# Kernel optimization log

Hardware: AMD Instinct MI355X
Metric: run time of the kernel (lower is better)

Reference implementation:

```python
import jax, jax.numpy as jnp
import numpy as np
import math

D_MODEL = 1024
NUM_HEADS = 16
D_K = D_MODEL // NUM_HEADS
SEQ_LEN = 2048
THETA = 10000.0


def _rope_tables(seq_len, d_k, theta):
    # inv_freq over even dims, angles repeated-interleaved to full d_k
    inv_freq = theta ** (-jnp.arange(0, d_k, 2, dtype=jnp.float32) / d_k)  # [d_k/2]
    pos = jnp.arange(seq_len, dtype=jnp.float32)                          # [s]
    angles = pos[:, None] * inv_freq[None, :]                             # [s, d_k/2]
    angles = jnp.repeat(angles, 2, axis=-1)                               # [s, d_k]
    return jnp.cos(angles), jnp.sin(angles)


def _rotate_half(x):
    # interleaved pairs: (x0,x1,x2,x3,...) -> (-x1,x0,-x3,x2,...)
    x_even = x[..., ::2]
    x_odd = x[..., 1::2]
    return jnp.stack([-x_odd, x_even], axis=-1).reshape(x.shape)


def _apply_rope(x, cos, sin):
    # x: [b, h, s, d_k]; cos/sin: [s, d_k]
    return x * cos + _rotate_half(x) * sin


def setup_inputs() -> dict:
    key = jax.random.key(0)
    ks = jax.random.split(key, 5)
    scale = 1.0 / math.sqrt(D_MODEL)
    X = jax.random.normal(ks[0], (2, SEQ_LEN, D_MODEL), dtype=jnp.float32)
    Wq = jax.random.normal(ks[1], (D_MODEL, D_MODEL), dtype=jnp.float32) * scale
    Wk = jax.random.normal(ks[2], (D_MODEL, D_MODEL), dtype=jnp.float32) * scale
    Wv = jax.random.normal(ks[3], (D_MODEL, D_MODEL), dtype=jnp.float32) * scale
    Wo = jax.random.normal(ks[4], (D_MODEL, D_MODEL), dtype=jnp.float32) * scale
    return {"X": X, "Wq": Wq, "Wk": Wk, "Wv": Wv, "Wo": Wo}


def reference(X, Wq, Wk, Wv, Wo):
    b, s, _ = X.shape
    h, dk = NUM_HEADS, D_K

    def proj(W):
        return (X @ W.T).reshape(b, s, h, dk).transpose(0, 2, 1, 3)  # [b,h,s,dk]

    q, k, v = proj(Wq), proj(Wk), proj(Wv)

    cos, sin = _rope_tables(s, dk, THETA)
    q = _apply_rope(q, cos, sin)
    k = _apply_rope(k, cos, sin)

    scores = jnp.einsum('bhid,bhjd->bhij', q, k) / math.sqrt(dk)
    causal = jnp.tril(jnp.ones((s, s), dtype=bool))
    scores = jnp.where(causal[None, None], scores, -jnp.inf)
    probs = jax.nn.softmax(scores, axis=-1)
    attended = jnp.einsum('bhij,bhjd->bhid', probs, v)               # [b,h,s,dk]

    out = attended.transpose(0, 2, 1, 3).reshape(b, s, h * dk)
    return out @ Wo.T
```

## Files before the change

### kernel.cpp

```cpp
#include <hip/hip_runtime.h>
#include <stdint.h>

#define D_MODEL 1024
#define NUM_HEADS 16
#define DK 64
#define SEQ 2048
#define BATCH 2
#define MROWS (BATCH * SEQ)
#define LOG2E 1.4426950408889634f
#define FIXM 14.0f

typedef short bf16x8 __attribute__((ext_vector_type(8)));
typedef float f32x4 __attribute__((ext_vector_type(4)));
typedef float f32x16 __attribute__((ext_vector_type(16)));

__device__ __forceinline__ unsigned short f2bf(float f) {
    unsigned int u = __float_as_uint(f);
    u = (u + 0x7fffu + ((u >> 16) & 1u)) >> 16;
    return (unsigned short)u;
}
__device__ __forceinline__ float bf2f(unsigned short h) {
    return __uint_as_float(((unsigned int)h) << 16);
}
__device__ __forceinline__ void async16(const void* g, void* l) {
    __builtin_amdgcn_global_load_lds(
        (const __attribute__((address_space(1))) void*)g,
        (__attribute__((address_space(3))) void*)l, 16, 0, 0);
}
__device__ __forceinline__ unsigned int cvtpk(float lo, float hi) {
    unsigned int r;
    asm("v_cvt_pk_bf16_f32 %0, %1, %2" : "=v"(r) : "v"(lo), "v"(hi));
    return r;
}
#define SWZ64(row, b) ((((row) * 8) + ((b) ^ ((row) & 7))) * 8)

__global__ void cast_all(const float4* __restrict__ X, const float4* __restrict__ Wq,
                         const float4* __restrict__ Wk, const float4* __restrict__ Wv,
                         const float4* __restrict__ Wo, ushort4* __restrict__ Xb,
                         ushort4* __restrict__ Wqkvb, ushort4* __restrict__ Wob) {
    int i = blockIdx.x * blockDim.x + threadIdx.x;
    const float4* src;
    ushort4* dst;
    int off;
    if (i < 1048576) { src = X; dst = Xb; off = i; }
    else if (i < 1310720) { src = Wq; dst = Wqkvb; off = i - 1048576; }
    else if (i < 1572864) { src = Wk; dst = Wqkvb + 262144; off = i - 1310720; }
    else if (i < 1835008) { src = Wv; dst = Wqkvb + 524288; off = i - 1572864; }
    else { src = Wo; dst = Wob; off = i - 1835008; }
    float4 v = src[off];
    ushort4 o;
    o.x = f2bf(v.x); o.y = f2bf(v.y); o.z = f2bf(v.z); o.w = f2bf(v.w);
    dst[off] = o;
}

template <int TN, int OUT_BF16>
__global__ __launch_bounds__(256) void gemm_tile(
    const unsigned short* __restrict__ A, const unsigned short* __restrict__ B,
    void* __restrict__ Cout, int M, int N, int K) {
    __shared__ unsigned short As[128 * 64];
    __shared__ unsigned short Bs[TN * 64];
    const int m0 = blockIdx.y * 128, n0 = blockIdx.x * TN;
    const int t = threadIdx.x;
    const int lane = t & 63, wave = t >> 6;
    const int mA = lane & 15, quad = lane >> 4;
    constexpr int MI = (TN == 128) ? 4 : 2;
    constexpr int NI = 4;
    const int wr = (TN == 128) ? (wave >> 1) * 64 : wave * 32;
    const int wc = (TN == 128) ? (wave & 1) * 64 : 0;

    f32x4 acc[MI][NI] = {};
    for (int k0 = 0; k0 < K; k0 += 64) {
#pragma unroll
        for (int i = 0; i < 4; ++i) {
            int ch = i * 256 + t;
            int r = ch >> 3, b = (ch & 7) ^ (r & 7);
            async16(A + (size_t)(m0 + r) * K + k0 + b * 8, (char*)As + ch * 16);
        }
#pragma unroll
        for (int i = 0; i < TN / 32; ++i) {
            int ch = i * 256 + t;
            int r = ch >> 3, b = (ch & 7) ^ (r & 7);
            async16(B + (size_t)(n0 + r) * K + k0 + b * 8, (char*)Bs + ch * 16);
        }
        __syncthreads();
#pragma unroll
        for (int kk = 0; kk < 2; ++kk) {
            bf16x8 af[MI], bfr[NI];
#pragma unroll
            for (int mi = 0; mi < MI; ++mi) {
                int rr = wr + mi * 16 + mA;
                af[mi] = *(const bf16x8*)&As[SWZ64(rr, kk * 4 + quad)];
            }
#pragma unroll
            for (int ni = 0; ni < NI; ++ni) {
                int rr = wc + ni * 16 + mA;
                bfr[ni] = *(const bf16x8*)&Bs[SWZ64(rr, kk * 4 + quad)];
            }
#pragma unroll
            for (int mi = 0; mi < MI; ++mi)
#pragma unroll
                for (int ni = 0; ni < NI; ++ni)
                    acc[mi][ni] = __builtin_amdgcn_mfma_f32_16x16x32_bf16(
                        af[mi], bfr[ni], acc[mi][ni], 0, 0, 0);
        }
        __syncthreads();
    }
#pragma unroll
    for (int mi = 0; mi < MI; ++mi)
#pragma unroll
        for (int ni = 0; ni < NI; ++ni)
#pragma unroll
            for (int r = 0; r < 4; ++r) {
                int gm = m0 + wr + mi * 16 + quad * 4 + r;
                int gn = n0 + wc + ni * 16 + mA;
                if (OUT_BF16)
                    ((unsigned short*)Cout)[(size_t)gm * N + gn] = f2bf(acc[mi][ni][r]);
                else
                    ((float*)Cout)[(size_t)gm * N + gn] = acc[mi][ni][r];
            }
}

__global__ __launch_bounds__(256) void rope_vt(const unsigned short* __restrict__ QKV,
                                               unsigned short* __restrict__ Qr,
                                               unsigned short* __restrict__ Kr,
                                               unsigned short* __restrict__ Vt) {
    __shared__ unsigned short T[64][80];
    const int bx = blockIdx.x;
    const int t = threadIdx.x;
    if (bx < 4096) {
        int tid = bx * 256 + t;
        int bs = tid >> 8;
        int p4 = tid & 255;
        int b = bs >> 11, spos = bs & 2047;
        int h = p4 >> 4, dd = (p4 & 15) * 4;
        float sn0, cs0, sn1, cs1;
        {
            float if0 = __expf(-(float)dd * (9.210340371976184f / 64.0f));
            float if1 = __expf(-(float)(dd + 2) * (9.210340371976184f / 64.0f));
            __sincosf((float)spos * if0, &sn0, &cs0);
            __sincosf((float)spos * if1, &sn1, &cs1);
        }
        const float SCQ = 0.125f * LOG2E;
        float cs0q = cs0 * SCQ, sn0q = sn0 * SCQ;
        float cs1q = cs1 * SCQ, sn1q = sn1 * SCQ;
        size_t src = (size_t)bs * 3072 + h * 64 + dd;
        ushort4 qw = *(const ushort4*)&QKV[src];
        ushort4 kw = *(const ushort4*)&QKV[src + 1024];
        ushort4 qo_, ko_;
        float e = bf2f(qw.x), o = bf2f(qw.y);
        qo_.x = f2bf(e * cs0q - o * sn0q); qo_.y = f2bf(o * cs0q + e * sn0q);
        e = bf2f(qw.z); o = bf2f(qw.w);
        qo_.z = f2bf(e * cs1q - o * sn1q); qo_.w = f2bf(o * cs1q + e * sn1q);
        e = bf2f(kw.x); o = bf2f(kw.y);
        ko_.x = f2bf(e * cs0 - o * sn0); ko_.y = f2bf(o * cs0 + e * sn0);
        e = bf2f(kw.z); o = bf2f(kw.w);
        ko_.z = f2bf(e * cs1 - o * sn1); ko_.w = f2bf(o * cs1 + e * sn1);
        size_t qb = (((size_t)(b * NUM_HEADS + h) * SEQ + spos) * DK + dd);
        *(ushort4*)&Qr[qb] = qo_;
        *(ushort4*)&Kr[qb] = ko_;
    } else {
        int idx = bx - 4096;
        const int s0 = (idx & 31) * 64, bh = idx >> 5;
        const int b = bh >> 4, h = bh & 15;
#pragma unroll
        for (int i = 0; i < 2; ++i) {
            int ch = i * 256 + t;
            int row = ch >> 3, bc = ch & 7;
            *(int4*)&T[row][bc * 8] =
                *(const int4*)&QKV[(size_t)(b * SEQ + s0 + row) * 3072 + 2048 + h * 64 + bc * 8];
        }
        __syncthreads();
#pragma unroll
        for (int i = 0; i < 2; ++i) {
            int ch = i * 256 + t;
            int d = ch >> 3, sb = ch & 7;
            unsigned short tmp[8];
#pragma unroll
            for (int j = 0; j < 8; ++j) tmp[j] = T[sb * 8 + j][d];
            *(int4*)&Vt[(size_t)bh * DK * SEQ + (size_t)d * SEQ + s0 + sb * 8] = *(int4*)tmp;
        }
    }
}

__global__ __launch_bounds__(256, 4) void flash_attn10(
    const unsigned short* __restrict__ Qr, const unsigned short* __restrict__ Kr,
    const unsigned short* __restrict__ Vt, unsigned short* __restrict__ Att) {
    __shared__ unsigned short Ks[2][64 * 64];
    __shared__ unsigned short Vs[2][64 * 64];
    const int bh = blockIdx.x;
    const int qt = 31 - (int)blockIdx.y;
    const int t = threadIdx.x;
    const int lane = t & 63, wave = t >> 6;
    const int l31 = lane & 31, lh = lane >> 5;
    const int wq = wave >> 1, wd = wave & 1;
    const size_t qkbase = (size_t)bh * SEQ * DK;
    const unsigned short* Kg = Kr + qkbase;
    const unsigned short* Vg = Vt + (size_t)bh * DK * SEQ;
    const int qg = qt * 64 + wq * 32 + l31;

    bf16x8 aq[4];
#pragma unroll
    for (int kk = 0; kk < 4; ++kk)
        aq[kk] = *(const bf16x8*)&Qr[qkbase + (size_t)qg * DK + kk * 16 + lh * 8];

    f32x16 acc0, acc1;
#pragma unroll
    for (int r = 0; r < 16; ++r) { acc0[r] = 0.f; acc1[r] = 0.f; }
    float la[4] = {0.f, 0.f, 0.f, 0.f};

#pragma unroll
    for (int i = 0; i < 2; ++i) {
        int ch = i * 256 + t;
        int row = ch >> 3, sb = (ch & 7) ^ (row & 7);
        async16(Kg + (size_t)row * DK + sb * 8, (char*)Ks[0] + ch * 16);
        async16(Vg + (size_t)row * SEQ + sb * 8, (char*)Vs[0] + ch * 16);
    }

    for (int jt = 0; jt <= qt; ++jt) {
        __syncthreads();
        const int cur = jt & 1;
        if (jt < qt) {
            const int j1 = (jt + 1) * 64;
#pragma unroll
            for (int i = 0; i < 2; ++i) {
                int ch = i * 256 + t;
                int row = ch >> 3, sb = (ch & 7) ^ (row & 7);
                async16(Kg + (size_t)(j1 + row) * DK + sb * 8, (char*)Ks[cur ^ 1] + ch * 16);
                async16(Vg + (size_t)row * SEQ + j1 + sb * 8, (char*)Vs[cur ^ 1] + ch * 16);
            }
        }
        const unsigned short* Kt = Ks[cur];
        const unsigned short* Vtile = Vs[cur];
        const bool diag = (jt == qt);
        if (diag && wd > wq) continue;

        f32x16 s;
#pragma unroll
        for (int r = 0; r < 16; ++r) s[r] = 0.f;
        __builtin_amdgcn_s_setprio(1);
#pragma unroll
        for (int kk = 0; kk < 4; ++kk) {
            bf16x8 kf = *(const bf16x8*)&Kt[SWZ64(wd * 32 + l31, kk * 2 + lh)];
            s = __builtin_amdgcn_mfma_f32_32x32x16_bf16(kf, aq[kk], s, 0, 0, 0);
        }
        __builtin_amdgcn_s_setprio(0);
        if (diag && wd == wq) {
#pragma unroll
            for (int r = 0; r < 16; ++r) {
                int crow = (r & 3) + 8 * (r >> 2) + 4 * lh;
                if (crow > l31) s[r] = -1e30f;
            }
        }

#pragma unroll
        for (int r = 0; r < 16; ++r) {
            s[r] = __builtin_amdgcn_exp2f(s[r] - FIXM);
            la[r & 3] += s[r];
        }

        bf16x8 frA, frB;
        {
            unsigned int u0 = cvtpk(s[0], s[1]), v0 = cvtpk(s[4], s[5]);
            unsigned int u1 = cvtpk(s[2], s[3]), v1 = cvtpk(s[6], s[7]);
            asm("v_permlane32_swap_b32 %0, %1" : "+v"(u0), "+v"(v0));
            asm("v_permlane32_swap_b32 %0, %1" : "+v"(u1), "+v"(v1));
            uint4 w = {u0, u1, v0, v1};
            frA = *(bf16x8*)&w;
            unsigned int u2 = cvtpk(s[8], s[9]), v2 = cvtpk(s[12], s[13]);
            unsigned int u3 = cvtpk(s[10], s[11]), v3 = cvtpk(s[14], s[15]);
            asm("v_permlane32_swap_b32 %0, %1" : "+v"(u2), "+v"(v2));
            asm("v_permlane32_swap_b32 %0, %1" : "+v"(u3), "+v"(v3));
            uint4 w2_ = {u2, u3, v2, v3};
            frB = *(bf16x8*)&w2_;
        }

        __builtin_amdgcn_s_setprio(1);
        {
            bf16x8 vf0 = *(const bf16x8*)&Vtile[SWZ64(l31, (wd * 2 + 0) * 2 + lh)];
            acc0 = __builtin_amdgcn_mfma_f32_32x32x16_bf16(vf0, frA, acc0, 0, 0, 0);
            bf16x8 vf1 = *(const bf16x8*)&Vtile[SWZ64(l31, (wd * 2 + 1) * 2 + lh)];
            acc0 = __builtin_amdgcn_mfma_f32_32x32x16_bf16(vf1, frB, acc0, 0, 0, 0);
            bf16x8 vf2 = *(const bf16x8*)&Vtile[SWZ64(32 + l31, (wd * 2 + 0) * 2 + lh)];
            acc1 = __builtin_amdgcn_mfma_f32_32x32x16_bf16(vf2, frA, acc1, 0, 0, 0);
            bf16x8 vf3 = *(const bf16x8*)&Vtile[SWZ64(32 + l31, (wd * 2 + 1) * 2 + lh)];
            acc1 = __builtin_amdgcn_mfma_f32_32x32x16_bf16(vf3, frB, acc1, 0, 0, 0);
        }
        __builtin_amdgcn_s_setprio(0);
    }

    float lt = (la[0] + la[1]) + (la[2] + la[3]);
    lt += __shfl_xor(lt, 32, 64);
    __syncthreads();
    float* SC = (float*)Ks;
    float* LS = (float*)Vs;
    if (wd == 0) {
#pragma unroll
        for (int r = 0; r < 16; ++r) SC[(wq * 2 + 1) * 1024 + r * 64 + lane] = acc1[r];
    } else {
#pragma unroll
        for (int r = 0; r < 16; ++r) SC[(wq * 2 + 0) * 1024 + r * 64 + lane] = acc0[r];
    }
    if (lane < 32) LS[wave * 32 + l31] = lt;
    __syncthreads();
    const float rl = 1.0f / (LS[(wq * 2) * 32 + l31] + LS[(wq * 2 + 1) * 32 + l31]);
    float outv[16];
    if (wd == 0) {
#pragma unroll
        for (int r = 0; r < 16; ++r)
            outv[r] = acc0[r] + SC[(wq * 2 + 0) * 1024 + r * 64 + lane];
    } else {
#pragma unroll
        for (int r = 0; r < 16; ++r)
            outv[r] = acc1[r] + SC[(wq * 2 + 1) * 1024 + r * 64 + lane];
    }

    const int b_ = bh >> 4, h_ = bh & 15;
#pragma unroll
    for (int rg = 0; rg < 4; ++rg) {
        ushort4 o;
        o.x = f2bf(outv[rg * 4 + 0] * rl);
        o.y = f2bf(outv[rg * 4 + 1] * rl);
        o.z = f2bf(outv[rg * 4 + 2] * rl);
        o.w = f2bf(outv[rg * 4 + 3] * rl);
        *(ushort4*)&Att[(size_t)(b_ * SEQ + qg) * D_MODEL + h_ * DK + wd * 32 + 8 * rg + 4 * lh] = o;
    }
}

extern "C" void kernel_launch(void* const* d_in, const int* in_sizes, int n_in,
                              void* d_out, int out_size, void* d_ws, size_t ws_size,
                              hipStream_t stream) {
    const float* X = (const float*)d_in[0];
    const float* Wq = (const float*)d_in[1];
    const float* Wk = (const float*)d_in[2];
    const float* Wv = (const float*)d_in[3];
    const float* Wo = (const float*)d_in[4];

    char* ws = (char*)d_ws;
    unsigned short* Xb     = (unsigned short*)(ws + 0);
    unsigned short* Wqkvb  = (unsigned short*)(ws + (8u << 20));
    unsigned short* Wob    = (unsigned short*)(ws + (14u << 20));
    unsigned short* QKVraw = (unsigned short*)(ws + (16u << 20));
    unsigned short* Kr     = (unsigned short*)(ws + (40u << 20));
    unsigned short* Vt     = (unsigned short*)(ws + (48u << 20));
    unsigned short* Qr     = Xb;
    unsigned short* Att    = QKVraw;

    cast_all<<<8192, 256, 0, stream>>>((const float4*)X, (const float4*)Wq,
                                       (const float4*)Wk, (const float4*)Wv,
                                       (const float4*)Wo, (ushort4*)Xb,
                                       (ushort4*)Wqkvb, (ushort4*)Wob);

    gemm_tile<128, 1><<<dim3(3072 / 128, MROWS / 128), 256, 0, stream>>>(
        Xb, Wqkvb, QKVraw, MROWS, 3072, D_MODEL);

    rope_vt<<<4096 + 1024, 256, 0, stream>>>(QKVraw, Qr, Kr, Vt);

    flash_attn10<<<dim3(BATCH * NUM_HEADS, 32), 256, 0, stream>>>(Qr, Kr, Vt, Att);

    gemm_tile<64, 0><<<dim3(D_MODEL / 64, MROWS / 128), 256, 0, stream>>>(
        Att, Wob, d_out, MROWS, D_MODEL, D_MODEL);
}
```

Baseline: 175.0 us.

## Switch GEMM tiles to 32x32x16 MFMA and add XCD-aware block swizzle

Both projection GEMMs now use 32x32x16 bf16 MFMA instructions instead of 16x16x32. This changes the fragment loads, the accumulator layout and the epilogue indexing. The block index is also remapped across groups of 8 so that neighbouring tiles land on the same XCD, aiming for better L2 reuse. The larger MFMA cuts LDS reads per flop and the instruction count. The swizzle assumes the workgroup count is divisible by 8.

```diff
diff --git a/kernel.cpp b/kernel.cpp
--- a/kernel.cpp
+++ b/kernel.cpp
@@ -54,21 +54,31 @@
 }
 
 template <int TN, int OUT_BF16>
-__global__ __launch_bounds__(256) void gemm_tile(
+__global__ __launch_bounds__(256) void gemm_tile32(
     const unsigned short* __restrict__ A, const unsigned short* __restrict__ B,
     void* __restrict__ Cout, int M, int N, int K) {
     __shared__ unsigned short As[128 * 64];
     __shared__ unsigned short Bs[TN * 64];
-    const int m0 = blockIdx.y * 128, n0 = blockIdx.x * TN;
+    const int nwg = gridDim.x * gridDim.y;
+    const int bid = blockIdx.y * gridDim.x + blockIdx.x;
+    const int swz = (bid & 7) * (nwg >> 3) + (bid >> 3);
+    const int m0 = (swz / gridDim.x) * 128, n0 = (swz % gridDim.x) * TN;
     const int t = threadIdx.x;
     const int lane = t & 63, wave = t >> 6;
-    const int mA = lane & 15, quad = lane >> 4;
-    constexpr int MI = (TN == 128) ? 4 : 2;
-    constexpr int NI = 4;
+    const int l31 = lane & 31, lh = lane >> 5;
+    constexpr int MI = (TN == 128) ? 2 : 1;
+    constexpr int NI = 2;
     const int wr = (TN == 128) ? (wave >> 1) * 64 : wave * 32;
     const int wc = (TN == 128) ? (wave & 1) * 64 : 0;
 
-    f32x4 acc[MI][NI] = {};
+    f32x16 acc[MI][NI];
+#pragma unroll
+    for (int mi = 0; mi < MI; ++mi)
+#pragma unroll
+        for (int ni = 0; ni < NI; ++ni)
+#pragma unroll
+            for (int r = 0; r < 16; ++r) acc[mi][ni][r] = 0.f;
+
     for (int k0 = 0; k0 < K; k0 += 64) {
 #pragma unroll
         for (int i = 0; i < 4; ++i) {
@@ -84,23 +94,19 @@
         }
         __syncthreads();
 #pragma unroll
-        for (int kk = 0; kk < 2; ++kk) {
+        for (int ks = 0; ks < 4; ++ks) {
             bf16x8 af[MI], bfr[NI];
 #pragma unroll
-            for (int mi = 0; mi < MI; ++mi) {
-                int rr = wr + mi * 16 + mA;
-                af[mi] = *(const bf16x8*)&As[SWZ64(rr, kk * 4 + quad)];
-            }
-#pragma unroll
-            for (int ni = 0; ni < NI; ++ni) {
-                int rr = wc + ni * 16 + mA;
-                bfr[ni] = *(const bf16x8*)&Bs[SWZ64(rr, kk * 4 + quad)];
-            }
-#pragma unroll
             for (int mi = 0; mi < MI; ++mi)
+                af[mi] = *(const bf16x8*)&As[SWZ64(wr + mi * 32 + l31, ks * 2 + lh)];
+#pragma unroll
+            for (int ni = 0; ni < NI; ++ni)
+                bfr[ni] = *(const bf16x8*)&Bs[SWZ64(wc + ni * 32 + l31, ks * 2 + lh)];
+#pragma unroll
+            for (int mi = 0; mi < MI; ++mi)
 #pragma unroll
                 for (int ni = 0; ni < NI; ++ni)
-                    acc[mi][ni] = __builtin_amdgcn_mfma_f32_16x16x32_bf16(
+                    acc[mi][ni] = __builtin_amdgcn_mfma_f32_32x32x16_bf16(
                         af[mi], bfr[ni], acc[mi][ni], 0, 0, 0);
         }
         __syncthreads();
@@ -110,14 +116,17 @@
 #pragma unroll
         for (int ni = 0; ni < NI; ++ni)
 #pragma unroll
-            for (int r = 0; r < 4; ++r) {
-                int gm = m0 + wr + mi * 16 + quad * 4 + r;
-                int gn = n0 + wc + ni * 16 + mA;
-                if (OUT_BF16)
-                    ((unsigned short*)Cout)[(size_t)gm * N + gn] = f2bf(acc[mi][ni][r]);
-                else
-                    ((float*)Cout)[(size_t)gm * N + gn] = acc[mi][ni][r];
-            }
+            for (int rg = 0; rg < 4; ++rg)
+#pragma unroll
+                for (int c = 0; c < 4; ++c) {
+                    int gm = m0 + wr + mi * 32 + 8 * rg + 4 * lh + c;
+                    int gn = n0 + wc + ni * 32 + l31;
+                    float v = acc[mi][ni][rg * 4 + c];
+                    if (OUT_BF16)
+                        ((unsigned short*)Cout)[(size_t)gm * N + gn] = f2bf(v);
+                    else
+                        ((float*)Cout)[(size_t)gm * N + gn] = v;
+                }
 }
 
 __global__ __launch_bounds__(256) void rope_vt(const unsigned short* __restrict__ QKV,
@@ -350,13 +359,13 @@
                                        (const float4*)Wo, (ushort4*)Xb,
                                        (ushort4*)Wqkvb, (ushort4*)Wob);
 
-    gemm_tile<128, 1><<<dim3(3072 / 128, MROWS / 128), 256, 0, stream>>>(
+    gemm_tile32<128, 1><<<dim3(3072 / 128, MROWS / 128), 256, 0, stream>>>(
         Xb, Wqkvb, QKVraw, MROWS, 3072, D_MODEL);
 
     rope_vt<<<4096 + 1024, 256, 0, stream>>>(QKVraw, Qr, Kr, Vt);
 
     flash_attn10<<<dim3(BATCH * NUM_HEADS, 32), 256, 0, stream>>>(Qr, Kr, Vt, Att);
 
-    gemm_tile<64, 0><<<dim3(D_MODEL / 64, MROWS / 128), 256, 0, stream>>>(
+    gemm_tile32<64, 0><<<dim3(D_MODEL / 64, MROWS / 128), 256, 0, stream>>>(
         Att, Wob, d_out, MROWS, D_MODEL, D_MODEL);
 }
```

Measured after the change: 173.1 us. Within noise of the previous version (-1.1%).
